# Kernel optimization log

Hardware: AMD Instinct MI355X
Metric: run time of the kernel (lower is better)

The kernel has to match this reference:

```python
import jax, jax.numpy as jnp
import numpy as np

N_HEADS = 32
N_KV_HEADS = 8
HEAD_DIM = 64
D_MODEL = 2048
SLIDING_WINDOW = 512
ROPE_THETA = 10000.0
PAST_LENGTH = 0
EPS = 1e-6


def setup_inputs() -> dict:
    key = jax.random.key(0)
    k1, k2, k3 = jax.random.split(key, 3)
    B, S = 1, 2048
    q_size = N_HEADS * HEAD_DIM
    kv_size = N_KV_HEADS * HEAD_DIM
    return {
        "x": jax.random.normal(k1, (B, S, D_MODEL), dtype=jnp.float32),
        "w_qkv": jax.random.normal(k2, (q_size + 2 * kv_size, D_MODEL), dtype=jnp.float32) * (D_MODEL ** -0.5),
        "w_out": jax.random.normal(k3, (D_MODEL, q_size), dtype=jnp.float32) * (q_size ** -0.5),
        "q_norm_w": jnp.ones((HEAD_DIM,), dtype=jnp.float32),
        "k_norm_w": jnp.ones((HEAD_DIM,), dtype=jnp.float32),
    }


def _rms_norm(x, w):
    xf = x.astype(jnp.float32)
    rms = jax.lax.rsqrt(jnp.mean(xf * xf, axis=-1, keepdims=True) + EPS)
    return (xf * rms).astype(x.dtype) * w


def _rope(q, k, past_length):
    # q: [b, h, s, d], k: [b, kv, s, d]
    s, d = q.shape[2], q.shape[3]
    inv_freq = 1.0 / (ROPE_THETA ** (jnp.arange(0, d, 2, dtype=jnp.float32) / d))
    pos = jnp.arange(s, dtype=jnp.float32) + past_length
    ang = pos[:, None] * inv_freq[None, :]            # [s, d/2]
    emb = jnp.concatenate([ang, ang], axis=-1)        # [s, d]
    cos, sin = jnp.cos(emb), jnp.sin(emb)

    def rot_half(x):
        x1, x2 = jnp.split(x, 2, axis=-1)
        return jnp.concatenate([-x2, x1], axis=-1)

    q = q * cos + rot_half(q) * sin
    k = k * cos + rot_half(k) * sin
    return q, k


def _sliding_mask(seq_len, total_len, past_length):
    q_idx = jnp.arange(seq_len)[:, None]
    k_idx = jnp.arange(total_len)[None, :]
    causal = (q_idx + past_length) >= k_idx
    window = (q_idx + past_length - k_idx) < SLIDING_WINDOW
    keep = causal & window
    return jnp.where(keep, 0.0, -jnp.inf).astype(jnp.float32)[None, None]


def reference(x, w_qkv, w_out, q_norm_w, k_norm_w):
    b, s, _ = x.shape
    n_rep = N_HEADS // N_KV_HEADS
    q_size = N_HEADS * HEAD_DIM
    kv_size = N_KV_HEADS * HEAD_DIM

    qkv = jnp.einsum('bsd,od->bso', x, w_qkv)
    q, k, v = jnp.split(qkv, [q_size, q_size + kv_size], axis=-1)
    q = q.reshape(b, s, N_HEADS, HEAD_DIM).transpose(0, 2, 1, 3)
    k = k.reshape(b, s, N_KV_HEADS, HEAD_DIM).transpose(0, 2, 1, 3)
    v = v.reshape(b, s, N_KV_HEADS, HEAD_DIM).transpose(0, 2, 1, 3)

    q = _rms_norm(q, q_norm_w)
    k = _rms_norm(k, k_norm_w)
    q, k = _rope(q, k, PAST_LENGTH)

    k_rep = jnp.repeat(k, n_rep, axis=1)  # [b, H, s, d]
    v_rep = jnp.repeat(v, n_rep, axis=1)

    scale = HEAD_DIM ** -0.5
    scores = jnp.einsum('bhqd,bhkd->bhqk', q, k_rep) * scale
    scores = scores + _sliding_mask(s, s, PAST_LENGTH)
    probs = jax.nn.softmax(scores, axis=-1)
    attn = jnp.einsum('bhqk,bhkd->bhqd', probs, v_rep)

    attn = attn.transpose(0, 2, 1, 3).reshape(b, s, q_size)
    return jnp.einsum('bso,do->bsd', attn, w_out)
```

## Files before the change

### kernel.cpp

```cpp
#include <hip/hip_runtime.h>

typedef unsigned short u16;
typedef unsigned int u32;
typedef __bf16 bf16x8 __attribute__((ext_vector_type(8)));
typedef float f32x4 __attribute__((ext_vector_type(4)));
typedef float f32x16 __attribute__((ext_vector_type(16)));
typedef u16 u16x8 __attribute__((ext_vector_type(8)));
typedef u32 u32x2 __attribute__((ext_vector_type(2)));
typedef u32 u32x4 __attribute__((ext_vector_type(4)));

#define MFMA16(a, b, c) __builtin_amdgcn_mfma_f32_16x16x32_bf16((a), (b), (c), 0, 0, 0)
#define MFMA32(a, b, c) __builtin_amdgcn_mfma_f32_32x32x16_bf16((a), (b), (c), 0, 0, 0)

__device__ __forceinline__ u16 f2bf(float f) {
    unsigned int u = __float_as_uint(f);
    u = (u + 0x7FFF + ((u >> 16) & 1)) >> 16;
    return (u16)u;
}

__device__ __forceinline__ float bf2f(u16 v) {
    return __uint_as_float(((u32)v) << 16);
}

__device__ __forceinline__ u32 cvtpk(float a, float b) {
    u32 d;
    asm("v_cvt_pk_bf16_f32 %0, %1, %2" : "=v"(d) : "v"(a), "v"(b));
    return d;
}

__device__ __forceinline__ void gld_lds16(const u16* g, u16* l) {
    __builtin_amdgcn_global_load_lds(
        (const __attribute__((address_space(1))) unsigned int*)g,
        (__attribute__((address_space(3))) unsigned int*)l, 16, 0, 0);
}

__global__ __launch_bounds__(256) void cvt2_bf16(const float* __restrict__ in1,
                                                 u16* __restrict__ out1, int n41,
                                                 const float* __restrict__ in2,
                                                 u16* __restrict__ out2, int n42) {
    int idx = blockIdx.x * blockDim.x + threadIdx.x;
    int stride = gridDim.x * blockDim.x;
    for (int i = idx; i < n41; i += stride) {
        float4 v = reinterpret_cast<const float4*>(in1)[i];
        ushort4 o;
        o.x = f2bf(v.x); o.y = f2bf(v.y); o.z = f2bf(v.z); o.w = f2bf(v.w);
        reinterpret_cast<ushort4*>(out1)[i] = o;
    }
    for (int i = idx; i < n42; i += stride) {
        float4 v = reinterpret_cast<const float4*>(in2)[i];
        ushort4 o;
        o.x = f2bf(v.x); o.y = f2bf(v.y); o.z = f2bf(v.z); o.w = f2bf(v.w);
        reinterpret_cast<ushort4*>(out2)[i] = o;
    }
}

__global__ __launch_bounds__(256) void reduce_add(const float4* __restrict__ a,
                                                  const float4* __restrict__ b,
                                                  float4* __restrict__ o, int n4) {
    int idx = blockIdx.x * blockDim.x + threadIdx.x;
    int stride = gridDim.x * blockDim.x;
    for (int i = idx; i < n4; i += stride) {
        float4 va = a[i], vb = b[i];
        float4 vo = {va.x + vb.x, va.y + vb.y, va.z + vb.z, va.w + vb.w};
        o[i] = vo;
    }
}

template <int SPLITK, int RM, int RN, int XN, bool OBF16>
__global__ __launch_bounds__(512) void gemm_bt(const u16* __restrict__ A,
                                               const u16* __restrict__ B,
                                               void* __restrict__ Cv,
                                               int M, int N, int K) {
    __shared__ __align__(16) u16 As[3][128 * 32];
    __shared__ __align__(16) u16 Bs[3][256 * 32];

    int bid = blockIdx.x;
    int xcd = bid & 7;
    int r = bid >> 3;
    int tm = (xcd / XN) * RM + (r / RN);
    int tn = (xcd % XN) * RN + (r % RN);
    int m0 = tm << 7, n0 = tn << 8;

    int Ks = K / SPLITK;
    int kbase = blockIdx.y * Ks;

    int t = threadIdx.x;
    int w = t >> 6, l = t & 63, lrow = l & 15, lhi = l >> 4;
    int wr = w >> 2, wc = w & 3;

    int rowA = t >> 2;
    int col0 = (((t & 3) ^ ((t >> 3) & 3)) << 3);

    const u16* Ag = A + (size_t)m0 * K + kbase;
    const u16* Bg = B + (size_t)n0 * K + kbase;

    auto stage = [&](int sbuf, int kt) {
        int k0 = kt << 5;
        gld_lds16(Ag + (size_t)rowA * K + k0 + col0, &As[sbuf][t * 8]);
        gld_lds16(Bg + (size_t)rowA * K + k0 + col0, &Bs[sbuf][t * 8]);
        gld_lds16(Bg + (size_t)(rowA + 128) * K + k0 + col0, &Bs[sbuf][t * 8 + 4096]);
    };

    f32x4 acc[4][4] = {};
    int NT = Ks >> 5;
    stage(0, 0); stage(1, 1); stage(2, 2);
    asm volatile("s_waitcnt vmcnt(6)" ::: "memory");
    asm volatile("s_barrier" ::: "memory");
    int cur = 0;
    for (int kt = 0; kt < NT; ++kt) {
        bf16x8 af[4], bfr[4];
#pragma unroll
        for (int i = 0; i < 4; ++i) {
            int row = wr * 64 + i * 16 + lrow;
            af[i] = *(const bf16x8*)&As[cur][row * 32 + ((lhi ^ ((row >> 1) & 3)) << 3)];
        }
#pragma unroll
        for (int j = 0; j < 4; ++j) {
            int row = wc * 64 + j * 16 + lrow;
            bfr[j] = *(const bf16x8*)&Bs[cur][row * 32 + ((lhi ^ ((row >> 1) & 3)) << 3)];
        }
        asm volatile("s_waitcnt lgkmcnt(0)" ::: "memory");
        __builtin_amdgcn_sched_barrier(0);
        asm volatile("s_barrier" ::: "memory");
        if (kt + 3 < NT) stage(cur, kt + 3);
#pragma unroll
        for (int i = 0; i < 4; ++i)
#pragma unroll
            for (int j = 0; j < 4; ++j)
                acc[i][j] = MFMA16(af[i], bfr[j], acc[i][j]);
        if (kt + 1 < NT) {
            if (kt + 3 < NT)      asm volatile("s_waitcnt vmcnt(6)" ::: "memory");
            else if (kt + 2 < NT) asm volatile("s_waitcnt vmcnt(3)" ::: "memory");
            else                  asm volatile("s_waitcnt vmcnt(0)" ::: "memory");
            asm volatile("s_barrier" ::: "memory");
        }
        cur = (cur == 2) ? 0 : cur + 1;
    }
#pragma unroll
    for (int i = 0; i < 4; ++i) {
#pragma unroll
        for (int j = 0; j < 4; ++j) {
            int crow = m0 + wr * 64 + i * 16 + lhi * 4;
            int ccol = n0 + wc * 64 + j * 16 + lrow;
            if (OBF16) {
                u16* cp = (u16*)Cv + (size_t)blockIdx.y * ((size_t)M * N)
                                   + (size_t)crow * N + ccol;
#pragma unroll
                for (int r2 = 0; r2 < 4; ++r2) cp[(size_t)r2 * N] = f2bf(acc[i][j][r2]);
            } else {
                float* cp = (float*)Cv + (size_t)blockIdx.y * ((size_t)M * N)
                                       + (size_t)crow * N + ccol;
#pragma unroll
                for (int r2 = 0; r2 < 4; ++r2) cp[(size_t)r2 * N] = acc[i][j][r2];
            }
        }
    }
}

__global__ __launch_bounds__(256) void qkv_post(const u16* __restrict__ qkv0,
                                                const u16* __restrict__ qkv1,
                                                const float* __restrict__ qw,
                                                const float* __restrict__ kw,
                                                u16* __restrict__ qb,
                                                u16* __restrict__ kb,
                                                u16* __restrict__ vb) {
    const float C = 0.18033688011112042f;
    int s = blockIdx.x;
    int t = threadIdx.x, w = t >> 6, lane = t & 63;
    const u16* row0 = qkv0 + (size_t)s * 3072;
    const u16* row1 = qkv1 + (size_t)s * 3072;
    int d2 = lane & 31;
    float inv = exp2f(-(float)d2 * (13.287712379549449f / 32.0f));
    float ang = (float)s * inv;
    float cs = cosf(ang), sn = sinf(ang);
    for (int h = w; h < 48; h += 4) {
        float v = bf2f(row0[h * 64 + lane]) + bf2f(row1[h * 64 + lane]);
        if (h < 40) {
            float ss = v * v;
#pragma unroll
            for (int m = 32; m; m >>= 1) ss += __shfl_xor(ss, m);
            float rms = rsqrtf(ss * (1.0f / 64.0f) + 1e-6f);
            float wgt = (h < 32) ? qw[lane] : kw[lane];
            v = v * rms * wgt;
            float part = __shfl_xor(v, 32);
            float rot = (lane < 32) ? -part : part;
            v = v * cs + rot * sn;
            if (h < 32)
                qb[((size_t)h * 2048 + s) * 64 + lane] = f2bf(v * C);
            else
                kb[((size_t)(h - 32) * 2048 + s) * 64 + lane] = f2bf(v);
        } else {
            vb[((size_t)(h - 40) * 2048 + s) * 64 + lane] = f2bf(v);
        }
    }
}

__global__ __launch_bounds__(256) void transpose_v(const u16* __restrict__ vb,
                                                   u16* __restrict__ vt) {
    int kv = blockIdx.y;
    int s0 = blockIdx.x * 256;
    __shared__ __align__(16) u16 tile[64][256];
    int t = threadIdx.x;
    int sl = t >> 3;
    int d0 = (t & 7) * 8;
#pragma unroll
    for (int j = 0; j < 8; ++j) {
        int s = sl + j * 32;
        u16x8 v = *(const u16x8*)(vb + ((size_t)kv * 2048 + s0 + s) * 64 + d0);
#pragma unroll
        for (int e = 0; e < 8; ++e) tile[d0 + e][s] = v[e];
    }
    __syncthreads();
    int d = t >> 2;
    int so = (t & 3) * 64;
#pragma unroll
    for (int j = 0; j < 8; ++j) {
        int s_local = so + j * 8;
        *(u16x8*)(vt + ((size_t)kv * 64 + d) * 2048 + s0 + s_local) =
            *(const u16x8*)&tile[d][s_local];
    }
}

__global__ __launch_bounds__(256) void attn_fa10(const u16* __restrict__ qb,
                                                 const u16* __restrict__ kb,
                                                 const u16* __restrict__ vt,
                                                 u16* __restrict__ ab,
                                                 const float* __restrict__ wout,
                                                 u16* __restrict__ wb2) {
    int bid = blockIdx.x;
    if (bid >= 512) {
        int idx = (bid - 512) * 256 + threadIdx.x;
        int stride = 128 * 256;
        for (int i = idx; i < 2048 * 2048 / 4; i += stride) {
            float4 v = reinterpret_cast<const float4*>(wout)[i];
            ushort4 o;
            o.x = f2bf(v.x); o.y = f2bf(v.y); o.z = f2bf(v.z); o.w = f2bf(v.w);
            reinterpret_cast<ushort4*>(wb2)[i] = o;
        }
        return;
    }
    int qt = bid & 15, h = bid >> 4, kv = h >> 2;
    int t = threadIdx.x, w = t >> 6, l = t & 63;
    int lq = l & 31, hi = l >> 5;
    int qlo_blk = qt * 128;
    int qlo = qlo_blk + w * 32;

    __shared__ __align__(16) u16 pool[32768];
    u16* KtA = pool;
    u16* KtB = pool + 8192;
    u16* VtA = pool + 16384;
    u16* VtB = pool + 24576;

    const u16* qrow = qb + ((size_t)h * 2048 + qlo + lq) * 64 + hi * 8;
    bf16x8 qf[4];
#pragma unroll
    for (int dk = 0; dk < 4; ++dk) qf[dk] = *(const bf16x8*)(qrow + dk * 16);

    f32x16 oa = {}, ob = {};
    float lsum = 0.f;

    int kstart = qlo_blk - 511; if (kstart < 0) kstart = 0;
    int ktA = kstart >> 7;
    int ktB = qlo_blk >> 7;
    const u16* kb_h = kb + (size_t)kv * 2048 * 64;
    const u16* vt_h = vt + (size_t)kv * 64 * 2048;

    auto stage = [&](u16* Kbuf, u16* Vbuf, int kt) {
        int k0 = kt << 7;
#pragma unroll
        for (int n = 0; n < 4; ++n) {
            int c = t + n * 256;
            int kr = c >> 3, kc = c & 7;
            gld_lds16(kb_h + (size_t)(k0 + kr) * 64 + ((kc ^ (kr & 7)) << 3),
                      Kbuf + c * 8);
            int vr = c >> 4, vc = c & 15;
            gld_lds16(vt_h + (size_t)vr * 2048 + k0 + ((vc ^ (vr & 15)) << 3),
                      Vbuf + c * 8);
        }
    };

    u16 *Kc = KtA, *Kn = KtB, *Vc = VtA, *Vn = VtB;
    stage(Kc, Vc, ktA);
    for (int kt = ktA; kt <= ktB; ++kt) {
        if (kt < ktB) {
            stage(Kn, Vn, kt + 1);
            asm volatile("s_waitcnt vmcnt(8)" ::: "memory");
        } else {
            asm volatile("s_waitcnt vmcnt(0)" ::: "memory");
        }
        asm volatile("s_barrier" ::: "memory");

        int k0 = kt << 7;
        int vswz = lq & 15;
#pragma unroll
        for (int pp = 0; pp < 2; ++pp) {
            int g0 = pp * 2, g1 = pp * 2 + 1;
            int k00 = k0 + g0 * 32, k01 = k0 + g1 * 32;
            bool act0 = (k00 <= qlo + 31) && (k00 + 31 >= qlo - 511);
            bool act1 = (k01 <= qlo + 31) && (k01 + 31 >= qlo - 511);
            if (!(act0 || act1)) continue;

            int kr0 = g0 * 32 + lq, kr1 = g1 * 32 + lq;
            int sz0 = kr0 & 7, sz1 = kr1 & 7;
            bf16x8 ka0 = *(const bf16x8*)&Kc[kr0 * 64 + (((0 + hi) ^ sz0) << 3)];
            bf16x8 ka1 = *(const bf16x8*)&Kc[kr0 * 64 + (((2 + hi) ^ sz0) << 3)];
            bf16x8 ka2 = *(const bf16x8*)&Kc[kr0 * 64 + (((4 + hi) ^ sz0) << 3)];
            bf16x8 ka3 = *(const bf16x8*)&Kc[kr0 * 64 + (((6 + hi) ^ sz0) << 3)];
            bf16x8 kb0 = *(const bf16x8*)&Kc[kr1 * 64 + (((0 + hi) ^ sz1) << 3)];
            bf16x8 kb1 = *(const bf16x8*)&Kc[kr1 * 64 + (((2 + hi) ^ sz1) << 3)];
            bf16x8 kb2 = *(const bf16x8*)&Kc[kr1 * 64 + (((4 + hi) ^ sz1) << 3)];
            bf16x8 kb3 = *(const bf16x8*)&Kc[kr1 * 64 + (((6 + hi) ^ sz1) << 3)];
            asm volatile("s_waitcnt lgkmcnt(0)" ::: "memory");
            __builtin_amdgcn_sched_barrier(0);

            f32x16 s0 = {}, s1 = {};
            s0 = MFMA32(ka0, qf[0], s0);  s1 = MFMA32(kb0, qf[0], s1);
            s0 = MFMA32(ka1, qf[1], s0);  s1 = MFMA32(kb1, qf[1], s1);
            s0 = MFMA32(ka2, qf[2], s0);  s1 = MFMA32(kb2, qf[2], s1);
            s0 = MFMA32(ka3, qf[3], s0);  s1 = MFMA32(kb3, qf[3], s1);

            bf16x8 va[2][2], vbl[2][2];
#pragma unroll
            for (int vi = 0; vi < 2; ++vi) {
                int c0 = ((g0 * 4 + vi * 2 + hi) ^ vswz) << 3;
                int c1 = ((g1 * 4 + vi * 2 + hi) ^ vswz) << 3;
                va[0][vi]  = *(const bf16x8*)&Vc[lq * 128 + c0];
                vbl[0][vi] = *(const bf16x8*)&Vc[(lq + 32) * 128 + c0];
                va[1][vi]  = *(const bf16x8*)&Vc[lq * 128 + c1];
                vbl[1][vi] = *(const bf16x8*)&Vc[(lq + 32) * 128 + c1];
            }

            int q = qlo + lq;
            bool edge0 = (k00 + 31 > qlo) || (qlo + 31 - k00 >= 512);
            if (edge0) {
#pragma unroll
                for (int r = 0; r < 16; ++r) {
                    int k = k00 + (r & 3) + 8 * (r >> 2) + 4 * hi;
                    if (!((unsigned)(q - k) < 512u)) s0[r] = -1e30f;
                }
            }
            bool edge1 = (k01 + 31 > qlo) || (qlo + 31 - k01 >= 512);
            if (edge1) {
#pragma unroll
                for (int r = 0; r < 16; ++r) {
                    int k = k01 + (r & 3) + 8 * (r >> 2) + 4 * hi;
                    if (!((unsigned)(q - k) < 512u)) s1[r] = -1e30f;
                }
            }

            float p0[16], p1[16];
#pragma unroll
            for (int r = 0; r < 16; ++r) {
                p0[r] = exp2f(s0[r]);
                p1[r] = exp2f(s1[r]);
                lsum += p0[r] + p1[r];
            }

            u32 a0 = cvtpk(p0[0], p0[1]),   a1 = cvtpk(p0[2], p0[3]);
            u32 a2 = cvtpk(p0[4], p0[5]),   a3 = cvtpk(p0[6], p0[7]);
            u32 a4 = cvtpk(p0[8], p0[9]),   a5 = cvtpk(p0[10], p0[11]);
            u32 a6 = cvtpk(p0[12], p0[13]), a7 = cvtpk(p0[14], p0[15]);
            u32 c0 = cvtpk(p1[0], p1[1]),   c1 = cvtpk(p1[2], p1[3]);
            u32 c2 = cvtpk(p1[4], p1[5]),   c3 = cvtpk(p1[6], p1[7]);
            u32 c4 = cvtpk(p1[8], p1[9]),   c5 = cvtpk(p1[10], p1[11]);
            u32 c6 = cvtpk(p1[12], p1[13]), c7 = cvtpk(p1[14], p1[15]);
            u32x2 ra02 = __builtin_amdgcn_permlane32_swap(a0, a2, false, false);
            u32x2 ra13 = __builtin_amdgcn_permlane32_swap(a1, a3, false, false);
            u32x2 ra46 = __builtin_amdgcn_permlane32_swap(a4, a6, false, false);
            u32x2 ra57 = __builtin_amdgcn_permlane32_swap(a5, a7, false, false);
            u32x2 rc02 = __builtin_amdgcn_permlane32_swap(c0, c2, false, false);
            u32x2 rc13 = __builtin_amdgcn_permlane32_swap(c1, c3, false, false);
            u32x2 rc46 = __builtin_amdgcn_permlane32_swap(c4, c6, false, false);
            u32x2 rc57 = __builtin_amdgcn_permlane32_swap(c5, c7, false, false);
            bf16x8 b0g0, b1g0, b0g1, b1g1;
            {
                u32* bp = (u32*)&b0g0;
                bp[0] = ra02[0]; bp[1] = ra13[0]; bp[2] = ra02[1]; bp[3] = ra13[1];
                u32* bq = (u32*)&b1g0;
                bq[0] = ra46[0]; bq[1] = ra57[0]; bq[2] = ra46[1]; bq[3] = ra57[1];
                u32* cp = (u32*)&b0g1;
                cp[0] = rc02[0]; cp[1] = rc13[0]; cp[2] = rc02[1]; cp[3] = rc13[1];
                u32* cq = (u32*)&b1g1;
                cq[0] = rc46[0]; cq[1] = rc57[0]; cq[2] = rc46[1]; cq[3] = rc57[1];
            }

            oa = MFMA32(va[0][0], b0g0, oa);  ob = MFMA32(vbl[0][0], b0g0, ob);
            oa = MFMA32(va[0][1], b1g0, oa);  ob = MFMA32(vbl[0][1], b1g0, ob);
            oa = MFMA32(va[1][0], b0g1, oa);  ob = MFMA32(vbl[1][0], b0g1, ob);
            oa = MFMA32(va[1][1], b1g1, oa);  ob = MFMA32(vbl[1][1], b1g1, ob);
        }
        asm volatile("s_barrier" ::: "memory");
        u16* tk = Kc; Kc = Kn; Kn = tk;
        u16* tv = Vc; Vc = Vn; Vn = tv;
    }

    u16* smw = pool + w * (32 * 66);
    lsum += __shfl_xor(lsum, 32);
    float inv = 1.0f / lsum;
#pragma unroll
    for (int rp = 0; rp < 8; ++rp) {
        int r = rp * 2;
        int d = (r & 3) + 8 * (r >> 2) + 4 * hi;
        *(u32*)&smw[lq * 66 + d]      = cvtpk(oa[r] * inv, oa[r + 1] * inv);
        *(u32*)&smw[lq * 66 + d + 32] = cvtpk(ob[r] * inv, ob[r + 1] * inv);
    }
    asm volatile("s_waitcnt lgkmcnt(0)" ::: "memory");
    int qr = l >> 1, dbase = (l & 1) * 32;
    size_t orow = (size_t)(qlo + qr) * 2048 + h * 64 + dbase;
#pragma unroll
    for (int c2 = 0; c2 < 8; ++c2) {
        u32 w0 = *(const u32*)&smw[qr * 66 + dbase + c2 * 4];
        u32 w1 = *(const u32*)&smw[qr * 66 + dbase + c2 * 4 + 2];
        u32x2 val = { w0, w1 };
        *(u32x2*)(ab + orow + c2 * 4) = val;
    }
}

extern "C" void kernel_launch(void* const* d_in, const int* in_sizes, int n_in,
                              void* d_out, int out_size, void* d_ws, size_t ws_size,
                              hipStream_t stream) {
    const float* x     = (const float*)d_in[0];
    const float* w_qkv = (const float*)d_in[1];
    const float* w_out = (const float*)d_in[2];
    const float* qw    = (const float*)d_in[3];
    const float* kw    = (const float*)d_in[4];
    float* out = (float*)d_out;

    char* ws = (char*)d_ws;
    u16*   x_b    = (u16*)(ws);
    u16*   wB     = (u16*)(ws + 8388608);
    u16*   q_b    = (u16*)(ws);
    u16*   k_b    = (u16*)(ws + 8388608);
    u16*   v_b    = (u16*)(ws + 10485760);
    u16*   v_t    = (u16*)(ws + 12582912);
    u16*   P0     = (u16*)(ws + 20971520);
    float* O0     = (float*)(ws + 20971520);
    float* O1     = (float*)(ws + 37748736);
    u16*   attn_b = (u16*)(ws + 54525952);
    u16*   wB2    = (u16*)(ws + 62914560);

    cvt2_bf16<<<2048, 256, 0, stream>>>(x, x_b, 2048 * 2048 / 4,
                                        w_qkv, wB, 3072 * 2048 / 4);
    gemm_bt<2, 8, 3, 4, true><<<dim3(192, 2), 512, 0, stream>>>(
        x_b, wB, P0, 2048, 3072, 2048);
    qkv_post<<<2048, 256, 0, stream>>>(P0, P0 + (size_t)2048 * 3072, qw, kw,
                                       q_b, k_b, v_b);
    transpose_v<<<dim3(8, 8), 256, 0, stream>>>(v_b, v_t);
    attn_fa10<<<640, 256, 0, stream>>>(q_b, k_b, v_t, attn_b, w_out, wB2);
    gemm_bt<2, 4, 4, 2, false><<<dim3(128, 2), 512, 0, stream>>>(
        attn_b, wB2, O0, 2048, 2048, 2048);
    reduce_add<<<1024, 256, 0, stream>>>((const float4*)O0, (const float4*)O1,
                                         (float4*)out, 2048 * 2048 / 4);
}
```

Baseline: 127.0 us.

## Store split-K output partials in bf16 and raise wave priority around MFMA blocks

The output projection GEMM now writes its two split-K partial sums as bf16 rather than fp32, and the final reduce kernel reads bf16 and adds in fp32. This halves the traffic for writing and re-reading the partials. Separately, s_setprio brackets are placed around the MFMA sequences in the GEMM and attention kernels so waves issuing matrix ops get scheduling priority. The bf16 partials add rounding error to the final output.

```diff
diff --git a/kernel.cpp b/kernel.cpp
--- a/kernel.cpp
+++ b/kernel.cpp
@@ -54,22 +54,31 @@
     }
 }
 
-__global__ __launch_bounds__(256) void reduce_add(const float4* __restrict__ a,
-                                                  const float4* __restrict__ b,
-                                                  float4* __restrict__ o, int n4) {
+__global__ __launch_bounds__(256) void reduce_add_bf(const u16x8* __restrict__ a,
+                                                     const u16x8* __restrict__ b,
+                                                     float4* __restrict__ o, int n8) {
     int idx = blockIdx.x * blockDim.x + threadIdx.x;
     int stride = gridDim.x * blockDim.x;
-    for (int i = idx; i < n4; i += stride) {
-        float4 va = a[i], vb = b[i];
-        float4 vo = {va.x + vb.x, va.y + vb.y, va.z + vb.z, va.w + vb.w};
-        o[i] = vo;
-    }
-}
-
-template <int SPLITK, int RM, int RN, int XN, bool OBF16>
+    for (int i = idx; i < n8; i += stride) {
+        u16x8 va = a[i], vb = b[i];
+        float4 o0, o1;
+        o0.x = bf2f(va[0]) + bf2f(vb[0]);
+        o0.y = bf2f(va[1]) + bf2f(vb[1]);
+        o0.z = bf2f(va[2]) + bf2f(vb[2]);
+        o0.w = bf2f(va[3]) + bf2f(vb[3]);
+        o1.x = bf2f(va[4]) + bf2f(vb[4]);
+        o1.y = bf2f(va[5]) + bf2f(vb[5]);
+        o1.z = bf2f(va[6]) + bf2f(vb[6]);
+        o1.w = bf2f(va[7]) + bf2f(vb[7]);
+        o[i * 2] = o0;
+        o[i * 2 + 1] = o1;
+    }
+}
+
+template <int SPLITK, int RM, int RN, int XN>
 __global__ __launch_bounds__(512) void gemm_bt(const u16* __restrict__ A,
                                                const u16* __restrict__ B,
-                                               void* __restrict__ Cv,
+                                               u16* __restrict__ C,
                                                int M, int N, int K) {
     __shared__ __align__(16) u16 As[3][128 * 32];
     __shared__ __align__(16) u16 Bs[3][256 * 32];
@@ -123,11 +132,13 @@
         __builtin_amdgcn_sched_barrier(0);
         asm volatile("s_barrier" ::: "memory");
         if (kt + 3 < NT) stage(cur, kt + 3);
+        __builtin_amdgcn_s_setprio(1);
 #pragma unroll
         for (int i = 0; i < 4; ++i)
 #pragma unroll
             for (int j = 0; j < 4; ++j)
                 acc[i][j] = MFMA16(af[i], bfr[j], acc[i][j]);
+        __builtin_amdgcn_s_setprio(0);
         if (kt + 1 < NT) {
             if (kt + 3 < NT)      asm volatile("s_waitcnt vmcnt(6)" ::: "memory");
             else if (kt + 2 < NT) asm volatile("s_waitcnt vmcnt(3)" ::: "memory");
@@ -142,17 +153,9 @@
         for (int j = 0; j < 4; ++j) {
             int crow = m0 + wr * 64 + i * 16 + lhi * 4;
             int ccol = n0 + wc * 64 + j * 16 + lrow;
-            if (OBF16) {
-                u16* cp = (u16*)Cv + (size_t)blockIdx.y * ((size_t)M * N)
-                                   + (size_t)crow * N + ccol;
-#pragma unroll
-                for (int r2 = 0; r2 < 4; ++r2) cp[(size_t)r2 * N] = f2bf(acc[i][j][r2]);
-            } else {
-                float* cp = (float*)Cv + (size_t)blockIdx.y * ((size_t)M * N)
-                                       + (size_t)crow * N + ccol;
-#pragma unroll
-                for (int r2 = 0; r2 < 4; ++r2) cp[(size_t)r2 * N] = acc[i][j][r2];
-            }
+            u16* cp = C + (size_t)blockIdx.y * ((size_t)M * N) + (size_t)crow * N + ccol;
+#pragma unroll
+            for (int r2 = 0; r2 < 4; ++r2) cp[(size_t)r2 * N] = f2bf(acc[i][j][r2]);
         }
     }
 }
@@ -313,11 +316,13 @@
             asm volatile("s_waitcnt lgkmcnt(0)" ::: "memory");
             __builtin_amdgcn_sched_barrier(0);
 
+            __builtin_amdgcn_s_setprio(1);
             f32x16 s0 = {}, s1 = {};
             s0 = MFMA32(ka0, qf[0], s0);  s1 = MFMA32(kb0, qf[0], s1);
             s0 = MFMA32(ka1, qf[1], s0);  s1 = MFMA32(kb1, qf[1], s1);
             s0 = MFMA32(ka2, qf[2], s0);  s1 = MFMA32(kb2, qf[2], s1);
             s0 = MFMA32(ka3, qf[3], s0);  s1 = MFMA32(kb3, qf[3], s1);
+            __builtin_amdgcn_s_setprio(0);
 
             bf16x8 va[2][2], vbl[2][2];
 #pragma unroll
@@ -384,10 +389,12 @@
                 cq[0] = rc46[0]; cq[1] = rc57[0]; cq[2] = rc46[1]; cq[3] = rc57[1];
             }
 
+            __builtin_amdgcn_s_setprio(1);
             oa = MFMA32(va[0][0], b0g0, oa);  ob = MFMA32(vbl[0][0], b0g0, ob);
             oa = MFMA32(va[0][1], b1g0, oa);  ob = MFMA32(vbl[0][1], b1g0, ob);
             oa = MFMA32(va[1][0], b0g1, oa);  ob = MFMA32(vbl[1][0], b0g1, ob);
             oa = MFMA32(va[1][1], b1g1, oa);  ob = MFMA32(vbl[1][1], b1g1, ob);
+            __builtin_amdgcn_s_setprio(0);
         }
         asm volatile("s_barrier" ::: "memory");
         u16* tk = Kc; Kc = Kn; Kn = tk;
@@ -434,21 +441,21 @@
     u16*   v_b    = (u16*)(ws + 10485760);
     u16*   v_t    = (u16*)(ws + 12582912);
     u16*   P0     = (u16*)(ws + 20971520);
-    float* O0     = (float*)(ws + 20971520);
-    float* O1     = (float*)(ws + 37748736);
+    u16*   O0     = (u16*)(ws + 20971520);
+    u16*   O1     = (u16*)(ws + 29360128);
     u16*   attn_b = (u16*)(ws + 54525952);
     u16*   wB2    = (u16*)(ws + 62914560);
 
     cvt2_bf16<<<2048, 256, 0, stream>>>(x, x_b, 2048 * 2048 / 4,
                                         w_qkv, wB, 3072 * 2048 / 4);
-    gemm_bt<2, 8, 3, 4, true><<<dim3(192, 2), 512, 0, stream>>>(
+    gemm_bt<2, 8, 3, 4><<<dim3(192, 2), 512, 0, stream>>>(
         x_b, wB, P0, 2048, 3072, 2048);
     qkv_post<<<2048, 256, 0, stream>>>(P0, P0 + (size_t)2048 * 3072, qw, kw,
                                        q_b, k_b, v_b);
     transpose_v<<<dim3(8, 8), 256, 0, stream>>>(v_b, v_t);
     attn_fa10<<<640, 256, 0, stream>>>(q_b, k_b, v_t, attn_b, w_out, wB2);
-    gemm_bt<2, 4, 4, 2, false><<<dim3(128, 2), 512, 0, stream>>>(
+    gemm_bt<2, 4, 4, 2><<<dim3(128, 2), 512, 0, stream>>>(
         attn_b, wB2, O0, 2048, 2048, 2048);
-    reduce_add<<<1024, 256, 0, stream>>>((const float4*)O0, (const float4*)O1,
-                                         (float4*)out, 2048 * 2048 / 4);
-}
+    reduce_add_bf<<<1024, 256, 0, stream>>>((const u16x8*)O0, (const u16x8*)O1,
+                                            (float4*)out, 2048 * 2048 / 8);
+}
```

Result: no change. 126.9 us (-0.1%).
